# Performance work log

Measured on AMD Instinct MI355X. Metric: run time of the kernel, lower is better.

Reference implementation:

```python
import jax, jax.numpy as jnp
import numpy as np

B, T, C, H, L, V = 2, 1024, 768, 12, 12, 50257
D = C // H  # head size = 64
EPS = 1e-5


def _layer_norm(x, w, b):
    m = x.mean(-1, keepdims=True)
    v = x.var(-1, keepdims=True)
    return (x - m) * jax.lax.rsqrt(v + EPS) * w + b


def setup_inputs() -> dict:
    key = jax.random.key(0)
    ks = jax.random.split(key, 8)
    std = 0.02
    res_std = 0.02 * (2 * L) ** -0.5  # NANOGPT_SCALE_INIT
    rn = lambda k, shape, s: jax.random.normal(k, shape, jnp.float32) * s
    return dict(
        idx=jax.random.randint(ks[0], (B, T), 0, V),
        wte=rn(ks[1], (V, C), std),
        wpe=rn(ks[2], (T, C), std),
        ln1_w=jnp.ones((L, C), jnp.float32), ln1_b=jnp.zeros((L, C), jnp.float32),
        qkv_w=rn(ks[3], (L, C, 3 * C), std), qkv_b=jnp.zeros((L, 3 * C), jnp.float32),
        proj_w=rn(ks[4], (L, C, C), res_std), proj_b=jnp.zeros((L, C), jnp.float32),
        ln2_w=jnp.ones((L, C), jnp.float32), ln2_b=jnp.zeros((L, C), jnp.float32),
        fc_w=rn(ks[5], (L, C, 4 * C), std), fc_b=jnp.zeros((L, 4 * C), jnp.float32),
        fco_w=rn(ks[6], (L, 4 * C, C), res_std), fco_b=jnp.zeros((L, C), jnp.float32),
        lnf_w=jnp.ones((C,), jnp.float32), lnf_b=jnp.zeros((C,), jnp.float32),
    )


def reference(idx, wte, wpe, ln1_w, ln1_b, qkv_w, qkv_b, proj_w, proj_b,
              ln2_w, ln2_b, fc_w, fc_b, fco_w, fco_b, lnf_w, lnf_b):
    x = wte[idx] + wpe[:T]  # [B, T, C] tok + pos emb
    mask = jnp.tril(jnp.ones((T, T), bool))  # causal
    scale = 1.0 / np.sqrt(D).astype(np.float32)

    def block(x, p):
        l1w, l1b, qw, qb, pw, pb, l2w, l2b, fw, fb, fow, fob = p
        h = _layer_norm(x, l1w, l1b)
        qkv = h @ qw + qb  # [B, T, 3C]
        q, k, v = jnp.split(qkv, 3, axis=-1)
        q = q.reshape(B, T, H, D)
        k = k.reshape(B, T, H, D)
        v = v.reshape(B, T, H, D)
        att = jnp.einsum('bqhd,bkhd->bhqk', q, k) * scale
        att = jnp.where(mask, att, -jnp.inf)
        att = jax.nn.softmax(att, axis=-1)
        y = jnp.einsum('bhqk,bkhd->bqhd', att, v).reshape(B, T, C)
        x = x + y @ pw + pb
        h2 = _layer_norm(x, l2w, l2b)
        x = x + jax.nn.gelu(h2 @ fw + fb, approximate=True) @ fow + fob
        return x, None

    x, _ = jax.lax.scan(block, x, (ln1_w, ln1_b, qkv_w, qkv_b, proj_w, proj_b,
                                   ln2_w, ln2_b, fc_w, fc_b, fco_w, fco_b))
    x = _layer_norm(x, lnf_w, lnf_b)
    logits = x @ wte.T  # tied lm_head
    return logits
```

## Files before the change

kernel.cpp:

```cpp
#include <hip/hip_runtime.h>
#include <cmath>
#include <cstdint>

#define T_SEQ 1024
#define NH 12
#define NL 12
#define NV 50257
#define CD 768
#define M_ROWS 2048

typedef __bf16 bf16_t;
typedef __bf16 bf16x8 __attribute__((ext_vector_type(8)));
typedef float f32x4 __attribute__((ext_vector_type(4)));

__device__ __forceinline__ void gload16(const bf16_t* g, bf16_t* l) {
  __builtin_amdgcn_global_load_lds(
      (const __attribute__((address_space(1))) void*)g,
      (__attribute__((address_space(3))) void*)l, 16, 0, 0);
}

__global__ __launch_bounds__(256) void embed_k(const int* __restrict__ idx,
    const float* __restrict__ wte, const float* __restrict__ wpe,
    float* __restrict__ x) {
  int m = blockIdx.x;
  int t = m & (T_SEQ - 1);
  int tok = idx[m];
  const float* a = wte + (size_t)tok * CD;
  const float* p = wpe + (size_t)t * CD;
  float* xr = x + (size_t)m * CD;
  int c = threadIdx.x;
  xr[c]       = a[c]       + p[c];
  xr[c + 256] = a[c + 256] + p[c + 256];
  xr[c + 512] = a[c + 512] + p[c + 512];
}

__global__ __launch_bounds__(256) void cvt_k(const float* __restrict__ in,
    bf16_t* __restrict__ out, int n4) {
  int i = blockIdx.x * 256 + threadIdx.x;
  if (i < n4) {
    float4 v = ((const float4*)in)[i];
    bf16_t* o = out + (size_t)i * 4;
    o[0] = (bf16_t)v.x; o[1] = (bf16_t)v.y;
    o[2] = (bf16_t)v.z; o[3] = (bf16_t)v.w;
  }
}

__global__ __launch_bounds__(256) void transcvt_k(const float* __restrict__ W0,
    bf16_t* __restrict__ WT0, int K, int N) {
  const float* W = W0 + (size_t)blockIdx.z * K * N;
  bf16_t* WT = WT0 + (size_t)blockIdx.z * N * K;
  __shared__ float tl[32][33];
  int k0 = blockIdx.y * 32, n0 = blockIdx.x * 32;
  int j = threadIdx.x & 31, i0 = threadIdx.x >> 5;
  #pragma unroll
  for (int i = i0; i < 32; i += 8) tl[i][j] = W[(size_t)(k0 + i) * N + n0 + j];
  __syncthreads();
  #pragma unroll
  for (int i = i0; i < 32; i += 8)
    WT[(size_t)(n0 + i) * K + k0 + j] = (bf16_t)tl[j][i];
}

__global__ __launch_bounds__(256) void ln_k(const float* __restrict__ x,
    const float* __restrict__ w, const float* __restrict__ bi,
    bf16_t* __restrict__ out) {
  int row = blockIdx.x;
  const float* xr = x + (size_t)row * CD;
  int t = threadIdx.x;
  float v0 = xr[t], v1 = xr[t + 256], v2 = xr[t + 512];
  float s = v0 + v1 + v2;
  float ss = v0 * v0 + v1 * v1 + v2 * v2;
  #pragma unroll
  for (int o = 1; o < 64; o <<= 1) { s += __shfl_xor(s, o); ss += __shfl_xor(ss, o); }
  __shared__ float sh[8];
  int wid = t >> 6, lane = t & 63;
  if (lane == 0) { sh[wid] = s; sh[4 + wid] = ss; }
  __syncthreads();
  s  = sh[0] + sh[1] + sh[2] + sh[3];
  ss = sh[4] + sh[5] + sh[6] + sh[7];
  float mean = s * (1.f / CD);
  float var  = ss * (1.f / CD) - mean * mean;
  float rs = rsqrtf(var + 1e-5f);
  bf16_t* orow = out + (size_t)row * CD;
  orow[t]       = (bf16_t)((v0 - mean) * rs * w[t]       + bi[t]);
  orow[t + 256] = (bf16_t)((v1 - mean) * rs * w[t + 256] + bi[t + 256]);
  orow[t + 512] = (bf16_t)((v2 - mean) * rs * w[t + 512] + bi[t + 512]);
}

template <int BM, int BN, int EPI, bool SWAP, bool XSWZ>
__global__ __launch_bounds__(256) void gemm_bt(
    const bf16_t* __restrict__ A,
    const bf16_t* __restrict__ BT,
    const float* __restrict__ bias,
    const float* __restrict__ resid,
    void* __restrict__ out_p,
    int Mdim, int Ndim, int Kdim) {
  constexpr int MR = BM / 32, NR = BN / 32;
  __shared__ __align__(1024) bf16_t As[2][BM * 32];
  __shared__ __align__(1024) bf16_t Bs[2][BN * 32];
  const int t = threadIdx.x;
  const int wid = t >> 6, lane = t & 63;
  const int wm = wid >> 1, wn = wid & 1;
  int bx = blockIdx.x, by = blockIdx.y;
  if (XSWZ) {
    int gx = gridDim.x;
    int lin = by * gx + bx;
    int cpx = (gx * gridDim.y) >> 3;
    int swz = (lin & 7) * cpx + (lin >> 3);
    bx = swz % gx; by = swz / gx;
  }
  const int m0 = (SWAP ? bx : by) * BM;
  const int n0 = (SWAP ? by : bx) * BN;
  const int l15 = lane & 15, lhi = lane >> 4;

  const int srow = lane >> 2;
  const int schk = lane & 3;

  auto stage = [&](int buf, int kt) {
    #pragma unroll
    for (int i = 0; i < BM / 64; ++i) {
      int rbase = wid * (BM / 4) + i * 16;
      int r = rbase + srow;
      int c = schk ^ ((r >> 1) & 3);
      gload16(A + (size_t)(m0 + r) * Kdim + kt + c * 8, &As[buf][rbase * 32]);
    }
    #pragma unroll
    for (int i = 0; i < BN / 64; ++i) {
      int rbase = wid * (BN / 4) + i * 16;
      int r = rbase + srow;
      int nr = n0 + r; if (nr >= Ndim) nr = Ndim - 1;
      int c = schk ^ ((r >> 1) & 3);
      gload16(BT + (size_t)nr * Kdim + kt + c * 8, &Bs[buf][rbase * 32]);
    }
  };

  f32x4 acc[MR][NR] = {};

  stage(0, 0);
  __syncthreads();
  int cur = 0;
  for (int kt = 0; kt < Kdim; kt += 32) {
    if (kt + 32 < Kdim) stage(cur ^ 1, kt + 32);

    bf16x8 af[MR], bfr[NR];
    #pragma unroll
    for (int mm = 0; mm < MR; ++mm) {
      int ra = wm * (BM / 2) + mm * 16 + l15;
      af[mm] = *(const bf16x8*)&As[cur][ra * 32 + ((lhi ^ (ra >> 1)) & 3) * 8];
    }
    #pragma unroll
    for (int nn = 0; nn < NR; ++nn) {
      int rb = wn * (BN / 2) + nn * 16 + l15;
      bfr[nn] = *(const bf16x8*)&Bs[cur][rb * 32 + ((lhi ^ (rb >> 1)) & 3) * 8];
    }
    #pragma unroll
    for (int mm = 0; mm < MR; ++mm)
      #pragma unroll
      for (int nn = 0; nn < NR; ++nn)
        acc[mm][nn] = __builtin_amdgcn_mfma_f32_16x16x32_bf16(af[mm], bfr[nn], acc[mm][nn], 0, 0, 0);

    __syncthreads();
    cur ^= 1;
  }

  bf16_t* ob = (bf16_t*)out_p;
  float*  of = (float*)out_p;
  const int row0 = m0 + wm * (BM / 2);
  const int col0 = n0 + wn * (BN / 2);
  #pragma unroll
  for (int mm = 0; mm < MR; ++mm) {
    #pragma unroll
    for (int nn = 0; nn < NR; ++nn) {
      int col = col0 + nn * 16 + l15;
      if (col >= Ndim) continue;
      float bv = (EPI != 3) ? bias[col] : 0.f;
      #pragma unroll
      for (int r = 0; r < 4; ++r) {
        int row = row0 + mm * 16 + lhi * 4 + r;
        float v = acc[mm][nn][r] + bv;
        size_t o = (size_t)row * Ndim + col;
        if (EPI == 0) {
          ob[o] = (bf16_t)v;
        } else if (EPI == 1) {
          float u = v + 0.044715f * v * v * v;
          v = 0.5f * v * (1.f + tanhf(0.79788456080286536f * u));
          ob[o] = (bf16_t)v;
        } else if (EPI == 2) {
          of[o] = resid[o] + v;
        } else {
          of[o] = v;
        }
      }
    }
  }
}

__global__ __launch_bounds__(256) void vtrans_k(const bf16_t* __restrict__ qkv,
                                                bf16_t* __restrict__ VT) {
  __shared__ __align__(16) bf16_t tl[64 * 72];
  const int bh = blockIdx.y;
  const int t0 = blockIdx.x * 64;
  const int b = bh / NH, h = bh % NH;
  const int tid = threadIdx.x;
  const int row = tid >> 2;
  const int seg = (tid & 3) * 16;

  const bf16_t* src = qkv + (size_t)(b * T_SEQ + t0 + row) * (3 * CD) + 2 * CD + h * 64 + seg;
  bf16x8 v0 = *(const bf16x8*)src;
  bf16x8 v1 = *(const bf16x8*)(src + 8);
  #pragma unroll
  for (int j = 0; j < 8; ++j) tl[(seg + j) * 72 + row] = v0[j];
  #pragma unroll
  for (int j = 0; j < 8; ++j) tl[(seg + 8 + j) * 72 + row] = v1[j];
  __syncthreads();

  bf16_t* dst = VT + ((size_t)bh * 64 + row) * T_SEQ + t0 + seg;
  *(bf16x8*)dst       = *(const bf16x8*)&tl[row * 72 + seg];
  *(bf16x8*)(dst + 8) = *(const bf16x8*)&tl[row * 72 + seg + 8];
}

__global__ __launch_bounds__(64) void attn_k(const bf16_t* __restrict__ qkv,
                                             const bf16_t* __restrict__ VT,
                                             bf16_t* __restrict__ y) {
  __shared__ __align__(16) bf16_t Ps[16 * 40];
  const int lane = threadIdx.x;
  const int gw = blockIdx.x;
  const int qi = gw & 63;
  const int bh = gw >> 6;
  const int h = bh % NH, b = bh / NH;
  const bf16_t* Qbase = qkv + (size_t)b * T_SEQ * (3 * CD) + h * 64;
  const bf16_t* Kbase = Qbase + CD;
  const bf16_t* Vt = VT + (size_t)bh * 64 * T_SEQ;

  const int l15 = lane & 15, lhi = lane >> 4;
  const int q0 = qi * 16;

  bf16x8 aq[2];
  #pragma unroll
  for (int c = 0; c < 2; ++c)
    aq[c] = *(const bf16x8*)(Qbase + (size_t)(q0 + l15) * (3 * CD) + c * 32 + lhi * 8);

  f32x4 acc[4] = {};
  float m_[4], l_[4];
  #pragma unroll
  for (int r = 0; r < 4; ++r) { m_[r] = -INFINITY; l_[r] = 0.f; }

  const int qrow = q0 + lhi * 4;
  const int nt = (q0 + 47) / 32;
  for (int kt = 0; kt < nt; ++kt) {
    const int k0 = kt * 32;
    f32x4 s[2] = {};
    #pragma unroll
    for (int c = 0; c < 2; ++c) {
      #pragma unroll
      for (int kc = 0; kc < 2; ++kc) {
        bf16x8 bk = *(const bf16x8*)(Kbase + (size_t)(k0 + kc * 16 + l15) * (3 * CD) + c * 32 + lhi * 8);
        s[kc] = __builtin_amdgcn_mfma_f32_16x16x32_bf16(aq[c], bk, s[kc], 0, 0, 0);
      }
    }
    float mx[4];
    #pragma unroll
    for (int r = 0; r < 4; ++r) mx[r] = -INFINITY;
    #pragma unroll
    for (int kc = 0; kc < 2; ++kc) {
      const int kcol = k0 + kc * 16 + l15;
      #pragma unroll
      for (int r = 0; r < 4; ++r) {
        float sv = (kcol <= qrow + r) ? s[kc][r] * 0.125f : -INFINITY;
        s[kc][r] = sv;
        mx[r] = fmaxf(mx[r], sv);
      }
    }
    #pragma unroll
    for (int r = 0; r < 4; ++r) {
      mx[r] = fmaxf(mx[r], __shfl_xor(mx[r], 1));
      mx[r] = fmaxf(mx[r], __shfl_xor(mx[r], 2));
      mx[r] = fmaxf(mx[r], __shfl_xor(mx[r], 4));
      mx[r] = fmaxf(mx[r], __shfl_xor(mx[r], 8));
    }
    float al[4], rs[4];
    #pragma unroll
    for (int r = 0; r < 4; ++r) {
      float mn = fmaxf(m_[r], mx[r]);
      al[r] = __expf(m_[r] - mn);
      m_[r] = mn;
      float p0 = __expf(s[0][r] - mn);
      float p1 = __expf(s[1][r] - mn);
      s[0][r] = p0; s[1][r] = p1;
      rs[r] = p0 + p1;
    }
    #pragma unroll
    for (int r = 0; r < 4; ++r) {
      rs[r] += __shfl_xor(rs[r], 1);
      rs[r] += __shfl_xor(rs[r], 2);
      rs[r] += __shfl_xor(rs[r], 4);
      rs[r] += __shfl_xor(rs[r], 8);
      l_[r] = l_[r] * al[r] + rs[r];
    }
    #pragma unroll
    for (int dt = 0; dt < 4; ++dt)
      #pragma unroll
      for (int r = 0; r < 4; ++r) acc[dt][r] *= al[r];
    #pragma unroll
    for (int kc = 0; kc < 2; ++kc)
      #pragma unroll
      for (int r = 0; r < 4; ++r)
        Ps[(lhi * 4 + r) * 40 + kc * 16 + l15] = (bf16_t)s[kc][r];
    bf16x8 pa = *(const bf16x8*)&Ps[l15 * 40 + lhi * 8];
    #pragma unroll
    for (int dt = 0; dt < 4; ++dt) {
      bf16x8 bv = *(const bf16x8*)(Vt + (size_t)(dt * 16 + l15) * T_SEQ + k0 + lhi * 8);
      acc[dt] = __builtin_amdgcn_mfma_f32_16x16x32_bf16(pa, bv, acc[dt], 0, 0, 0);
    }
  }
  #pragma unroll
  for (int dt = 0; dt < 4; ++dt)
    #pragma unroll
    for (int r = 0; r < 4; ++r)
      y[(size_t)(b * T_SEQ + q0 + lhi * 4 + r) * CD + h * 64 + dt * 16 + l15] =
          (bf16_t)(acc[dt][r] / l_[r]);
}

extern "C" void kernel_launch(void* const* d_in, const int* in_sizes, int n_in,
                              void* d_out, int out_size, void* d_ws, size_t ws_size,
                              hipStream_t stream) {
  const int*   idx   = (const int*)d_in[0];
  const float* wte   = (const float*)d_in[1];
  const float* wpe   = (const float*)d_in[2];
  const float* ln1w  = (const float*)d_in[3];
  const float* ln1b  = (const float*)d_in[4];
  const float* qkvw  = (const float*)d_in[5];
  const float* qkvb  = (const float*)d_in[6];
  const float* projw = (const float*)d_in[7];
  const float* projb = (const float*)d_in[8];
  const float* ln2w  = (const float*)d_in[9];
  const float* ln2b  = (const float*)d_in[10];
  const float* fcw   = (const float*)d_in[11];
  const float* fcb   = (const float*)d_in[12];
  const float* fcow  = (const float*)d_in[13];
  const float* fcob  = (const float*)d_in[14];
  const float* lnfw  = (const float*)d_in[15];
  const float* lnfb  = (const float*)d_in[16];
  float* out = (float*)d_out;

  char* w = (char*)d_ws;
  auto alloc = [&](size_t bytes) {
    char* p = w; w += (bytes + 255) & ~(size_t)255; return p;
  };
  float*  x    = (float*)alloc((size_t)M_ROWS * CD * 4);
  float*  x2   = (float*)alloc((size_t)M_ROWS * CD * 4);
  bf16_t* hb   = (bf16_t*)alloc((size_t)M_ROWS * CD * 2);
  bf16_t* qkvB = (bf16_t*)alloc((size_t)M_ROWS * 3 * CD * 2);
  bf16_t* yb   = (bf16_t*)alloc((size_t)M_ROWS * CD * 2);
  bf16_t* fca  = (bf16_t*)alloc((size_t)M_ROWS * 4 * CD * 2);
  bf16_t* VT   = (bf16_t*)alloc((size_t)2 * NH * 64 * T_SEQ * 2);
  bf16_t* wteB = (bf16_t*)alloc((size_t)NV * CD * 2);
  bf16_t* wqT_s = (bf16_t*)alloc((size_t)3 * CD * CD * 2);
  bf16_t* wpT_s = (bf16_t*)alloc((size_t)CD * CD * 2);
  bf16_t* wfT_s = (bf16_t*)alloc((size_t)4 * CD * CD * 2);
  bf16_t* woT_s = (bf16_t*)alloc((size_t)CD * 4 * CD * 2);
  const size_t qkvSz = (size_t)3 * CD * CD, prSz = (size_t)CD * CD;
  const size_t fcSz  = (size_t)4 * CD * CD, foSz = (size_t)CD * 4 * CD;
  bf16_t* wqT_b = (bf16_t*)alloc(NL * qkvSz * 2);
  bf16_t* wpT_b = (bf16_t*)alloc(NL * prSz * 2);
  bf16_t* wfT_b = (bf16_t*)alloc(NL * fcSz * 2);
  bf16_t* woT_b = (bf16_t*)alloc(NL * foSz * 2);
  const bool big = (size_t)(w - (char*)d_ws) <= ws_size;

  embed_k<<<M_ROWS, 256, 0, stream>>>(idx, wte, wpe, x);
  {
    int n4 = NV * CD / 4;
    cvt_k<<<(n4 + 255) / 256, 256, 0, stream>>>(wte, wteB, n4);
  }
  if (big) {
    transcvt_k<<<dim3(3 * CD / 32, CD / 32, NL), 256, 0, stream>>>(qkvw,  wqT_b, CD, 3 * CD);
    transcvt_k<<<dim3(CD / 32, CD / 32, NL),     256, 0, stream>>>(projw, wpT_b, CD, CD);
    transcvt_k<<<dim3(4 * CD / 32, CD / 32, NL), 256, 0, stream>>>(fcw,   wfT_b, CD, 4 * CD);
    transcvt_k<<<dim3(CD / 32, 4 * CD / 32, NL), 256, 0, stream>>>(fcow,  woT_b, 4 * CD, CD);
  }

  for (int l = 0; l < NL; ++l) {
    bf16_t *wqT, *wpT, *wfT, *woT;
    if (big) {
      wqT = wqT_b + (size_t)l * qkvSz; wpT = wpT_b + (size_t)l * prSz;
      wfT = wfT_b + (size_t)l * fcSz;  woT = woT_b + (size_t)l * foSz;
    } else {
      wqT = wqT_s; wpT = wpT_s; wfT = wfT_s; woT = woT_s;
      transcvt_k<<<dim3(3 * CD / 32, CD / 32, 1), 256, 0, stream>>>(qkvw  + (size_t)l * CD * 3 * CD, wqT, CD, 3 * CD);
      transcvt_k<<<dim3(CD / 32, CD / 32, 1),     256, 0, stream>>>(projw + (size_t)l * CD * CD,     wpT, CD, CD);
      transcvt_k<<<dim3(4 * CD / 32, CD / 32, 1), 256, 0, stream>>>(fcw   + (size_t)l * CD * 4 * CD, wfT, CD, 4 * CD);
      transcvt_k<<<dim3(CD / 32, 4 * CD / 32, 1), 256, 0, stream>>>(fcow  + (size_t)l * 4 * CD * CD, woT, 4 * CD, CD);
    }

    ln_k<<<M_ROWS, 256, 0, stream>>>(x, ln1w + l * CD, ln1b + l * CD, hb);
    gemm_bt<128, 128, 0, false, false><<<dim3(3 * CD / 128, M_ROWS / 128), 256, 0, stream>>>(
        hb, wqT, qkvb + l * 3 * CD, nullptr, qkvB, M_ROWS, 3 * CD, CD);
    vtrans_k<<<dim3(T_SEQ / 64, 2 * NH), 256, 0, stream>>>(qkvB, VT);
    attn_k<<<2 * NH * 64, 64, 0, stream>>>(qkvB, VT, yb);
    gemm_bt<64, 64, 2, false, false><<<dim3(CD / 64, M_ROWS / 64), 256, 0, stream>>>(
        yb, wpT, projb + l * CD, x, x2, M_ROWS, CD, CD);
    ln_k<<<M_ROWS, 256, 0, stream>>>(x2, ln2w + l * CD, ln2b + l * CD, hb);
    gemm_bt<128, 128, 1, false, false><<<dim3(4 * CD / 128, M_ROWS / 128), 256, 0, stream>>>(
        hb, wfT, fcb + l * 4 * CD, nullptr, fca, M_ROWS, 4 * CD, CD);
    gemm_bt<64, 64, 2, false, false><<<dim3(CD / 64, M_ROWS / 64), 256, 0, stream>>>(
        fca, woT, fcob + l * CD, x2, x, M_ROWS, CD, 4 * CD);
  }

  ln_k<<<M_ROWS, 256, 0, stream>>>(x, lnfw, lnfb, hb);
  gemm_bt<128, 128, 3, true, true><<<dim3(M_ROWS / 128, (NV + 127) / 128), 256, 0, stream>>>(
      hb, wteB, nullptr, nullptr, out, M_ROWS, NV, CD);
}
```

Measured before the change: 2.517 ms.

## Add dedicated 256x256 LM-head GEMM and switch generic GEMM to K=64 single-buffer

Adds a specialized lm_head kernel with 256x256 tiles, 512 threads, double-buffered K=64 stages with explicit vmcnt waits, setprio around MFMA bursts, and a grouped block swizzle for L2 reuse of the large vocabulary matrix. The generic GEMM is changed from a double-buffered K=32 pipeline to a single-buffered K=64 tile with an 8-way XOR swizzle. This halves the number of barriers per K in the generic kernel, but global loads no longer overlap with compute there.

```diff
diff --git a/kernel.cpp b/kernel.cpp
--- a/kernel.cpp
+++ b/kernel.cpp
@@ -86,7 +86,7 @@
   orow[t + 512] = (bf16_t)((v2 - mean) * rs * w[t + 512] + bi[t + 512]);
 }
 
-template <int BM, int BN, int EPI, bool SWAP, bool XSWZ>
+template <int BM, int BN, int EPI>
 __global__ __launch_bounds__(256) void gemm_bt(
     const bf16_t* __restrict__ A,
     const bf16_t* __restrict__ BT,
@@ -95,71 +95,57 @@
     void* __restrict__ out_p,
     int Mdim, int Ndim, int Kdim) {
   constexpr int MR = BM / 32, NR = BN / 32;
-  __shared__ __align__(1024) bf16_t As[2][BM * 32];
-  __shared__ __align__(1024) bf16_t Bs[2][BN * 32];
+  __shared__ __align__(1024) bf16_t As[BM * 64];
+  __shared__ __align__(1024) bf16_t Bs[BN * 64];
   const int t = threadIdx.x;
   const int wid = t >> 6, lane = t & 63;
   const int wm = wid >> 1, wn = wid & 1;
-  int bx = blockIdx.x, by = blockIdx.y;
-  if (XSWZ) {
-    int gx = gridDim.x;
-    int lin = by * gx + bx;
-    int cpx = (gx * gridDim.y) >> 3;
-    int swz = (lin & 7) * cpx + (lin >> 3);
-    bx = swz % gx; by = swz / gx;
-  }
-  const int m0 = (SWAP ? bx : by) * BM;
-  const int n0 = (SWAP ? by : bx) * BN;
+  const int m0 = blockIdx.y * BM, n0 = blockIdx.x * BN;
   const int l15 = lane & 15, lhi = lane >> 4;
 
-  const int srow = lane >> 2;
-  const int schk = lane & 3;
-
-  auto stage = [&](int buf, int kt) {
-    #pragma unroll
-    for (int i = 0; i < BM / 64; ++i) {
-      int rbase = wid * (BM / 4) + i * 16;
+  const int srow = lane >> 3;
+  const int schk = lane & 7;
+
+  f32x4 acc[MR][NR] = {};
+
+  for (int kt = 0; kt < Kdim; kt += 64) {
+    #pragma unroll
+    for (int i = 0; i < BM / 32; ++i) {
+      int rbase = wid * (BM / 4) + i * 8;
       int r = rbase + srow;
-      int c = schk ^ ((r >> 1) & 3);
-      gload16(A + (size_t)(m0 + r) * Kdim + kt + c * 8, &As[buf][rbase * 32]);
-    }
-    #pragma unroll
-    for (int i = 0; i < BN / 64; ++i) {
-      int rbase = wid * (BN / 4) + i * 16;
+      int c = schk ^ (r & 7);
+      gload16(A + (size_t)(m0 + r) * Kdim + kt + c * 8, As + rbase * 64);
+    }
+    #pragma unroll
+    for (int i = 0; i < BN / 32; ++i) {
+      int rbase = wid * (BN / 4) + i * 8;
       int r = rbase + srow;
       int nr = n0 + r; if (nr >= Ndim) nr = Ndim - 1;
-      int c = schk ^ ((r >> 1) & 3);
-      gload16(BT + (size_t)nr * Kdim + kt + c * 8, &Bs[buf][rbase * 32]);
-    }
-  };
-
-  f32x4 acc[MR][NR] = {};
-
-  stage(0, 0);
-  __syncthreads();
-  int cur = 0;
-  for (int kt = 0; kt < Kdim; kt += 32) {
-    if (kt + 32 < Kdim) stage(cur ^ 1, kt + 32);
-
-    bf16x8 af[MR], bfr[NR];
-    #pragma unroll
-    for (int mm = 0; mm < MR; ++mm) {
-      int ra = wm * (BM / 2) + mm * 16 + l15;
-      af[mm] = *(const bf16x8*)&As[cur][ra * 32 + ((lhi ^ (ra >> 1)) & 3) * 8];
-    }
-    #pragma unroll
-    for (int nn = 0; nn < NR; ++nn) {
-      int rb = wn * (BN / 2) + nn * 16 + l15;
-      bfr[nn] = *(const bf16x8*)&Bs[cur][rb * 32 + ((lhi ^ (rb >> 1)) & 3) * 8];
-    }
-    #pragma unroll
-    for (int mm = 0; mm < MR; ++mm)
-      #pragma unroll
-      for (int nn = 0; nn < NR; ++nn)
-        acc[mm][nn] = __builtin_amdgcn_mfma_f32_16x16x32_bf16(af[mm], bfr[nn], acc[mm][nn], 0, 0, 0);
-
+      int c = schk ^ (r & 7);
+      gload16(BT + (size_t)nr * Kdim + kt + c * 8, Bs + rbase * 64);
+    }
     __syncthreads();
-    cur ^= 1;
+
+    #pragma unroll
+    for (int ks = 0; ks < 2; ++ks) {
+      bf16x8 af[MR], bfr[NR];
+      #pragma unroll
+      for (int mm = 0; mm < MR; ++mm) {
+        int ra = wm * (BM / 2) + mm * 16 + l15;
+        af[mm] = *(const bf16x8*)&As[ra * 64 + (((ks * 4 + lhi) ^ (ra & 7)) * 8)];
+      }
+      #pragma unroll
+      for (int nn = 0; nn < NR; ++nn) {
+        int rb = wn * (BN / 2) + nn * 16 + l15;
+        bfr[nn] = *(const bf16x8*)&Bs[rb * 64 + (((ks * 4 + lhi) ^ (rb & 7)) * 8)];
+      }
+      #pragma unroll
+      for (int mm = 0; mm < MR; ++mm)
+        #pragma unroll
+        for (int nn = 0; nn < NR; ++nn)
+          acc[mm][nn] = __builtin_amdgcn_mfma_f32_16x16x32_bf16(af[mm], bfr[nn], acc[mm][nn], 0, 0, 0);
+    }
+    __syncthreads();
   }
 
   bf16_t* ob = (bf16_t*)out_p;
@@ -189,6 +175,107 @@
         } else {
           of[o] = v;
         }
+      }
+    }
+  }
+}
+
+#define LM_NT 12
+#define LM_GY 197
+__global__ __launch_bounds__(512, 2) void gemm_lm(
+    const bf16_t* __restrict__ A,
+    const bf16_t* __restrict__ BT,
+    float* __restrict__ out) {
+  __shared__ __align__(1024) bf16_t As[2][256 * 64];
+  __shared__ __align__(1024) bf16_t Bs[2][256 * 64];
+  const int t = threadIdx.x;
+  const int wid = t >> 6, lane = t & 63;
+  const int wr = wid >> 2, wc = wid & 3;
+  const int l15 = lane & 15, lhi = lane >> 4;
+
+  int lin = blockIdx.x;
+  int swz = (lin & 7) * LM_GY + (lin >> 3);
+  const int m0 = (swz & 7) * 256;
+  const int n0 = (swz >> 3) * 256;
+
+  const int srow = lane >> 3;
+  const int csrc = ((lane & 7) ^ srow) * 8;
+
+  auto stage = [&](int buf, int kt) {
+    #pragma unroll
+    for (int i = 0; i < 4; ++i) {
+      int rb = i * 64 + wid * 8;
+      gload16(A + (size_t)(m0 + rb + srow) * CD + kt + csrc, &As[buf][rb * 64]);
+    }
+    #pragma unroll
+    for (int i = 0; i < 4; ++i) {
+      int rb = i * 64 + wid * 8;
+      int nr = n0 + rb + srow; if (nr >= NV) nr = NV - 1;
+      gload16(BT + (size_t)nr * CD + kt + csrc, &Bs[buf][rb * 64]);
+    }
+  };
+
+  f32x4 acc[8][4] = {};
+
+  stage(0, 0);
+  stage(1, 64);
+  for (int tt = 0; tt < LM_NT; ++tt) {
+    if (tt < LM_NT - 1) asm volatile("s_waitcnt vmcnt(8)" ::: "memory");
+    else                asm volatile("s_waitcnt vmcnt(0)" ::: "memory");
+    __builtin_amdgcn_sched_barrier(0);
+    __builtin_amdgcn_s_barrier();
+    __builtin_amdgcn_sched_barrier(0);
+
+    const bf16_t* Ab = As[tt & 1];
+    const bf16_t* Bb = Bs[tt & 1];
+    bf16x8 bfr[4][2];
+    #pragma unroll
+    for (int nn = 0; nn < 4; ++nn) {
+      int rb = wc * 64 + nn * 16 + l15;
+      #pragma unroll
+      for (int ks = 0; ks < 2; ++ks)
+        bfr[nn][ks] = *(const bf16x8*)&Bb[rb * 64 + (((ks * 4 + lhi) ^ (rb & 7)) * 8)];
+    }
+    #pragma unroll
+    for (int mh = 0; mh < 2; ++mh) {
+      bf16x8 af[4][2];
+      #pragma unroll
+      for (int mi = 0; mi < 4; ++mi) {
+        int ra = wr * 128 + (mh * 4 + mi) * 16 + l15;
+        #pragma unroll
+        for (int ks = 0; ks < 2; ++ks)
+          af[mi][ks] = *(const bf16x8*)&Ab[ra * 64 + (((ks * 4 + lhi) ^ (ra & 7)) * 8)];
+      }
+      __builtin_amdgcn_s_setprio(1);
+      #pragma unroll
+      for (int ks = 0; ks < 2; ++ks)
+        #pragma unroll
+        for (int mi = 0; mi < 4; ++mi)
+          #pragma unroll
+          for (int nn = 0; nn < 4; ++nn)
+            acc[mh * 4 + mi][nn] = __builtin_amdgcn_mfma_f32_16x16x32_bf16(
+                af[mi][ks], bfr[nn][ks], acc[mh * 4 + mi][nn], 0, 0, 0);
+      __builtin_amdgcn_s_setprio(0);
+    }
+
+    __builtin_amdgcn_sched_barrier(0);
+    __builtin_amdgcn_s_barrier();
+    __builtin_amdgcn_sched_barrier(0);
+    if (tt + 2 < LM_NT) stage(tt & 1, (tt + 2) * 64);
+  }
+
+  const int row0 = m0 + wr * 128;
+  const int col0 = n0 + wc * 64;
+  #pragma unroll
+  for (int mm = 0; mm < 8; ++mm) {
+    #pragma unroll
+    for (int nn = 0; nn < 4; ++nn) {
+      int col = col0 + nn * 16 + l15;
+      if (col >= NV) continue;
+      #pragma unroll
+      for (int r = 0; r < 4; ++r) {
+        int row = row0 + mm * 16 + lhi * 4 + r;
+        out[(size_t)row * NV + col] = acc[mm][nn][r];
       }
     }
   }
@@ -392,20 +479,19 @@
     }
 
     ln_k<<<M_ROWS, 256, 0, stream>>>(x, ln1w + l * CD, ln1b + l * CD, hb);
-    gemm_bt<128, 128, 0, false, false><<<dim3(3 * CD / 128, M_ROWS / 128), 256, 0, stream>>>(
+    gemm_bt<128, 128, 0><<<dim3(3 * CD / 128, M_ROWS / 128), 256, 0, stream>>>(
         hb, wqT, qkvb + l * 3 * CD, nullptr, qkvB, M_ROWS, 3 * CD, CD);
     vtrans_k<<<dim3(T_SEQ / 64, 2 * NH), 256, 0, stream>>>(qkvB, VT);
     attn_k<<<2 * NH * 64, 64, 0, stream>>>(qkvB, VT, yb);
-    gemm_bt<64, 64, 2, false, false><<<dim3(CD / 64, M_ROWS / 64), 256, 0, stream>>>(
+    gemm_bt<64, 64, 2><<<dim3(CD / 64, M_ROWS / 64), 256, 0, stream>>>(
         yb, wpT, projb + l * CD, x, x2, M_ROWS, CD, CD);
     ln_k<<<M_ROWS, 256, 0, stream>>>(x2, ln2w + l * CD, ln2b + l * CD, hb);
-    gemm_bt<128, 128, 1, false, false><<<dim3(4 * CD / 128, M_ROWS / 128), 256, 0, stream>>>(
+    gemm_bt<128, 128, 1><<<dim3(4 * CD / 128, M_ROWS / 128), 256, 0, stream>>>(
         hb, wfT, fcb + l * 4 * CD, nullptr, fca, M_ROWS, 4 * CD, CD);
-    gemm_bt<64, 64, 2, false, false><<<dim3(CD / 64, M_ROWS / 64), 256, 0, stream>>>(
+    gemm_bt<64, 64, 2><<<dim3(CD / 64, M_ROWS / 64), 256, 0, stream>>>(
         fca, woT, fcob + l * CD, x2, x, M_ROWS, CD, 4 * CD);
   }
 
   ln_k<<<M_ROWS, 256, 0, stream>>>(x, lnfw, lnfb, hb);
-  gemm_bt<128, 128, 3, true, true><<<dim3(M_ROWS / 128, (NV + 127) / 128), 256, 0, stream>>>(
-      hb, wteB, nullptr, nullptr, out, M_ROWS, NV, CD);
-}
+  gemm_lm<<<8 * LM_GY, 512, 0, stream>>>(hb, wteB, out);
+}
```

New measurement: 2.386 ms. 5.2% less time.

## Triple-buffer GEMM LDS staging with explicit vmcnt waits and MFMA priority

Applied to the files above, without the earlier changes.

The GEMM mainloop moves from a double-buffered LDS pipeline with a full __syncthreads per tile to a three-stage ring that prefetches two K-tiles ahead. Each iteration waits with a partial s_waitcnt vmcnt so only the oldest tile's loads must land, and it raises wave priority around the MFMA block. The aim is to hide global-load latency behind compute. In exchange, LDS use grows by half, which may lower occupancy for the 128x128 tiles, and the loop now relies on hand-placed barriers. The lm_head grid dimension is rewritten as a literal 16, which equals M_ROWS/128.

```diff
diff --git a/kernel.cpp b/kernel.cpp
--- a/kernel.cpp
+++ b/kernel.cpp
@@ -95,8 +95,9 @@
     void* __restrict__ out_p,
     int Mdim, int Ndim, int Kdim) {
   constexpr int MR = BM / 32, NR = BN / 32;
-  __shared__ __align__(1024) bf16_t As[2][BM * 32];
-  __shared__ __align__(1024) bf16_t Bs[2][BN * 32];
+  constexpr int LPW = (BM + BN) / 64;
+  __shared__ __align__(1024) bf16_t As[3][BM * 32];
+  __shared__ __align__(1024) bf16_t Bs[3][BN * 32];
   const int t = threadIdx.x;
   const int wid = t >> 6, lane = t & 63;
   const int wm = wid >> 1, wn = wid & 1;
@@ -115,13 +116,13 @@
   const int srow = lane >> 2;
   const int schk = lane & 3;
 
-  auto stage = [&](int buf, int kt) {
+  auto stage = [&](int bi, int kt) {
     #pragma unroll
     for (int i = 0; i < BM / 64; ++i) {
       int rbase = wid * (BM / 4) + i * 16;
       int r = rbase + srow;
       int c = schk ^ ((r >> 1) & 3);
-      gload16(A + (size_t)(m0 + r) * Kdim + kt + c * 8, &As[buf][rbase * 32]);
+      gload16(A + (size_t)(m0 + r) * Kdim + kt + c * 8, &As[bi][rbase * 32]);
     }
     #pragma unroll
     for (int i = 0; i < BN / 64; ++i) {
@@ -129,37 +130,48 @@
       int r = rbase + srow;
       int nr = n0 + r; if (nr >= Ndim) nr = Ndim - 1;
       int c = schk ^ ((r >> 1) & 3);
-      gload16(BT + (size_t)nr * Kdim + kt + c * 8, &Bs[buf][rbase * 32]);
+      gload16(BT + (size_t)nr * Kdim + kt + c * 8, &Bs[bi][rbase * 32]);
     }
   };
 
   f32x4 acc[MR][NR] = {};
+  const int NT = Kdim >> 5;
 
   stage(0, 0);
-  __syncthreads();
-  int cur = 0;
-  for (int kt = 0; kt < Kdim; kt += 32) {
-    if (kt + 32 < Kdim) stage(cur ^ 1, kt + 32);
-
+  if (NT > 1) stage(1, 32);
+  for (int tt = 0; tt < NT; ++tt) {
+    if (tt < NT - 1) asm volatile("s_waitcnt vmcnt(%0)" :: "i"(LPW) : "memory");
+    else             asm volatile("s_waitcnt vmcnt(0)" ::: "memory");
+    __builtin_amdgcn_sched_barrier(0);
+    __builtin_amdgcn_s_barrier();
+    __builtin_amdgcn_sched_barrier(0);
+
+    const bf16_t* Ab = As[tt % 3];
+    const bf16_t* Bb = Bs[tt % 3];
     bf16x8 af[MR], bfr[NR];
     #pragma unroll
     for (int mm = 0; mm < MR; ++mm) {
       int ra = wm * (BM / 2) + mm * 16 + l15;
-      af[mm] = *(const bf16x8*)&As[cur][ra * 32 + ((lhi ^ (ra >> 1)) & 3) * 8];
+      af[mm] = *(const bf16x8*)&Ab[ra * 32 + ((lhi ^ (ra >> 1)) & 3) * 8];
     }
     #pragma unroll
     for (int nn = 0; nn < NR; ++nn) {
       int rb = wn * (BN / 2) + nn * 16 + l15;
-      bfr[nn] = *(const bf16x8*)&Bs[cur][rb * 32 + ((lhi ^ (rb >> 1)) & 3) * 8];
-    }
+      bfr[nn] = *(const bf16x8*)&Bb[rb * 32 + ((lhi ^ (rb >> 1)) & 3) * 8];
+    }
+    if (tt + 2 < NT) stage((tt + 2) % 3, (tt + 2) * 32);
+
+    __builtin_amdgcn_s_setprio(1);
     #pragma unroll
     for (int mm = 0; mm < MR; ++mm)
       #pragma unroll
       for (int nn = 0; nn < NR; ++nn)
         acc[mm][nn] = __builtin_amdgcn_mfma_f32_16x16x32_bf16(af[mm], bfr[nn], acc[mm][nn], 0, 0, 0);
-
-    __syncthreads();
-    cur ^= 1;
+    __builtin_amdgcn_s_setprio(0);
+
+    __builtin_amdgcn_sched_barrier(0);
+    __builtin_amdgcn_s_barrier();
+    __builtin_amdgcn_sched_barrier(0);
   }
 
   bf16_t* ob = (bf16_t*)out_p;
@@ -406,6 +418,6 @@
   }
 
   ln_k<<<M_ROWS, 256, 0, stream>>>(x, lnfw, lnfb, hb);
-  gemm_bt<128, 128, 3, true, true><<<dim3(M_ROWS / 128, (NV + 127) / 128), 256, 0, stream>>>(
+  gemm_bt<128, 128, 3, true, true><<<dim3(16, (NV + 127) / 128), 256, 0, stream>>>(
       hb, wteB, nullptr, nullptr, out, M_ROWS, NV, CD);
 }
```

Measured after the change: 2.322 ms. 7.7% less time.
